# Performance work log

Hardware: AMD Instinct MI355X
Metric: run time of the kernel (lower is better)

Reference implementation:

```python
import jax, jax.numpy as jnp
import numpy as np
from jax import lax

B, D, H, W = 4, 32, 256, 256
ALPHA = 4.0     # init arg alpha
KFRAMES = 4.0   # self.K = alpha
EPS_BN = 1e-5

def FT2d(a):
    return jnp.fft.fft2(a, axes=(-2, -1))

def iFT2d(a):
    return jnp.fft.ifft2(a, axes=(-2, -1))

def forward_proj(field, otf):
    # field [B,D,H,W] real, otf [B,D,H,W] complex -> min-max scaled |holo| [B,1,H,W]
    Fholo = jnp.sum(FT2d(field.astype(jnp.complex64)) * otf, axis=1, keepdims=True)
    holo = jnp.abs(iFT2d(Fholo))
    mn = holo.min(axis=(-2, -1), keepdims=True)
    mx = holo.max(axis=(-2, -1), keepdims=True)
    return (holo - mn) / (mx - mn)

def back_proj(holo, otf):
    # holo [B,1,H,W] real -> real field [B,D,H,W]; broadcasting over depth == tile+FFT
    Fh = FT2d(holo.astype(jnp.complex64))
    return jnp.real(iFT2d(Fh * jnp.conj(otf)))

def cbl(xin, w, g, b, act):
    y = lax.conv_general_dilated(xin, w, (1, 1), 'SAME',
                                 dimension_numbers=('NCHW', 'OIHW', 'NCHW'))
    m = y.mean(axis=(0, 2, 3), keepdims=True)
    v = y.var(axis=(0, 2, 3), keepdims=True)  # biased var, torch BN training-mode
    y = (y - m) * lax.rsqrt(v + EPS_BN) * g[None, :, None, None] + b[None, :, None, None]
    return jax.nn.leaky_relu(y, 0.01) if act else y

def resblock(xin, wa, ga, ba, wb, gb, bb):
    h = cbl(cbl(xin, wa, ga, ba, True), wb, gb, bb, False)
    return jax.nn.leaky_relu(xin + h, 0.01)

def plholonet_forward(phi, z, u1, u2, otf, K1f, rho1, rho2, soft_thr, p):
    # ---- X update: FFT-domain proximal solve ----
    x1 = phi - u1
    x2 = z - u2
    n = rho1 * back_proj(x1, otf) + rho2 * x2
    d = (rho2 + jnp.abs(otf) ** 2 * rho1).astype(jnp.complex64)
    x = jnp.real(iFT2d(FT2d(n.astype(jnp.complex64)) / d))
    # ---- Phi update: vectorized 30-step masked bisection ----
    phi_tilde = forward_proj(x, otf) + u1
    K0 = 1.0 - K1f
    c = ALPHA / KFRAMES
    def func(y):
        return c * (K0 - K1f / (jnp.exp(c * y) - 1.0)) + rho1 * (y - phi_tilde)
    ind0_init = K1f == 0
    phimin = jnp.full_like(phi_tilde, 1e-5)
    phimax = jnp.full_like(phi_tilde, 100.0)
    phiave = 0.5 * (phimin + phimax)
    def step(carry, _):
        pmin, pmax, pave, ind0 = carry
        ind1 = jnp.logical_not(ind0)
        t = func(pave)
        pmin = jnp.where((t > 0) & ind1, pave, pmin)
        pmax = jnp.where((t < 0) & ind1, pave, pmax)
        ind0 = ind0 | ((t == 0) & ind1)
        pave = jnp.where(jnp.logical_not(ind0), 0.5 * (pmin + pmax), pave)
        return (pmin, pmax, pave, ind0), None
    (_, _, phiave, _), _ = lax.scan(step, (phimin, phimax, phiave, ind0_init), None, length=30)
    phi_next = jnp.where(ind0_init, phi_tilde - K0 / rho1, phiave)
    # ---- Z update: denoiser with symmetry loss ----
    z_tilde = x + u2
    h1 = resblock(z_tilde, p['w1a'], p['g1a'], p['b1a'], p['w1b'], p['g1b'], p['b1b'])
    h1_thr = jnp.sign(h1) * jax.nn.relu(jnp.abs(h1) - soft_thr)
    z_next = resblock(h1_thr, p['w2a'], p['g2a'], p['b2a'], p['w2b'], p['g2b'], p['b2b'])
    x_fb = resblock(h1, p['w2a'], p['g2a'], p['b2a'], p['w2b'], p['g2b'], p['b2b'])
    stage_symloss = x_fb - z_tilde
    # ---- dual updates ----
    u1_next = u1 + phi_next - forward_proj(x, otf)
    u2_next = u2 + z_next - x
    return (x, phi_next, z_next, u1_next, u2_next, stage_symloss)

def setup_inputs() -> dict:
    key = jax.random.key(0)
    ks = jax.random.split(key, 16)
    f = jnp.float32
    inp = dict(
        x=jax.random.normal(ks[0], (B, D, H, W), f),
        phi=jax.random.uniform(ks[1], (B, 1, H, W), dtype=f),
        z=jax.random.normal(ks[2], (B, D, H, W), f) * 0.1,
        u1=jax.random.uniform(ks[3], (B, 1, H, W), dtype=f) * 0.1,
        u2=jax.random.uniform(ks[4], (B, D, H, W), dtype=f) * 0.1,
        otf_real=jax.random.normal(ks[5], (B, D, H, W), f) * 0.5,
        otf_imag=jax.random.normal(ks[6], (B, D, H, W), f) * 0.5,
        K1=jax.random.randint(ks[7], (B, 1, H, W), 0, 5, jnp.int32),
        rho1=jnp.array([0.7], f),
        rho2=jnp.array([0.5], f),
        soft_thr=jnp.array([0.01], f),
    )
    for i, sfx in enumerate(['1a', '1b', '2a', '2b']):
        inp['w' + sfx] = jax.random.normal(ks[8 + i], (D, D, 3, 3), f) * 0.05
        inp['g' + sfx] = jnp.ones((D,), f)
        inp['b' + sfx] = jnp.zeros((D,), f)
    return inp

def reference(x, phi, z, u1, u2, otf_real, otf_imag, K1, rho1, rho2, soft_thr,
              w1a, g1a, b1a, w1b, g1b, b1b, w2a, g2a, b2a, w2b, g2b, b2b):
    # note: the torch forward immediately overwrites its `x` argument via X_update,
    # so the input x is unused (kept in the signature for interface faithfulness).
    otf = (otf_real + 1j * otf_imag).astype(jnp.complex64)
    K1f = K1.astype(jnp.float32)
    p = dict(w1a=w1a, g1a=g1a, b1a=b1a, w1b=w1b, g1b=g1b, b1b=b1b,
             w2a=w2a, g2a=g2a, b2a=b2a, w2b=w2b, g2b=g2b, b2b=b2b)
    return plholonet_forward(phi, z, u1, u2, otf, K1f, rho1, rho2, soft_thr, p)
```

## Files before the change

### kernel.cpp

```cpp
#include <hip/hip_runtime.h>
#include <math.h>

#define WDIM 256
#define HW   65536

struct cplx { float x, y; };
__device__ __forceinline__ cplx cmul(cplx a, cplx b){ return {a.x*b.x - a.y*b.y, a.x*b.y + a.y*b.x}; }
__device__ __forceinline__ cplx cadd(cplx a, cplx b){ return {a.x+b.x, a.y+b.y}; }
__device__ __forceinline__ cplx csub(cplx a, cplx b){ return {a.x-b.x, a.y-b.y}; }
__device__ __forceinline__ void swapc(cplx& a, cplx& b){ cplx t=a; a=b; b=t; }

typedef __attribute__((ext_vector_type(8))) short short8;
typedef __attribute__((ext_vector_type(4))) float float4v;

__device__ __forceinline__ unsigned short f2bf(float f){
  unsigned int u = __float_as_uint(f);
  unsigned int r = (u + 0x7FFFu + ((u >> 16) & 1u)) >> 16;
  return (unsigned short)r;
}
__device__ __forceinline__ float bf2f(unsigned short h){
  return __uint_as_float(((unsigned int)h) << 16);
}

template<bool INV>
__device__ __forceinline__ void fft16(cplx v[16]) {
  const float C16[8] = {1.f, 0.9238795325112867f, 0.7071067811865476f, 0.3826834323650898f,
                        0.f, -0.3826834323650898f, -0.7071067811865476f, -0.9238795325112867f};
  const float S16[8] = {0.f, 0.3826834323650898f, 0.7071067811865476f, 0.9238795325112867f,
                        1.f, 0.9238795325112867f, 0.7071067811865476f, 0.3826834323650898f};
  swapc(v[1], v[8]); swapc(v[2], v[4]); swapc(v[3], v[12]);
  swapc(v[5], v[10]); swapc(v[7], v[14]); swapc(v[11], v[13]);
  #pragma unroll
  for (int s = 1; s <= 4; ++s) {
    const int m = 1 << s, half = m >> 1, step = 16 >> s;
    #pragma unroll
    for (int k = 0; k < 16; k += m) {
      #pragma unroll
      for (int j = 0; j < half; ++j) {
        cplx w = {C16[j*step], INV ? S16[j*step] : -S16[j*step]};
        cplx t = cmul(w, v[k+j+half]);
        v[k+j+half] = csub(v[k+j], t);
        v[k+j]      = cadd(v[k+j], t);
      }
    }
  }
}

template<bool INV>
__device__ void fft256_16(cplx v[16], int t, cplx* Yu) {
  fft16<INV>(v);
  float ang = (INV ? 6.283185307179586f : -6.283185307179586f) * (float)t * (1.0f/256.0f);
  float sn, cs; sincosf(ang, &sn, &cs);
  cplx wstep = {cs, sn}, w = {1.f, 0.f};
  #pragma unroll
  for (int c = 0; c < 16; ++c) { v[c] = cmul(v[c], w); w = cmul(w, wstep); }
  __syncthreads();
  #pragma unroll
  for (int c = 0; c < 16; ++c) Yu[t*17 + c] = v[c];
  __syncthreads();
  cplx z[16];
  #pragma unroll
  for (int b = 0; b < 16; ++b) z[b] = Yu[b*17 + t];
  fft16<INV>(z);
  #pragma unroll
  for (int d = 0; d < 16; ++d) v[d] = z[d];
  __syncthreads();
}

__global__ __launch_bounds__(256) void k_row_fwd_sub(const float* __restrict__ a,
                                                     const float* __restrict__ b,
                                                     cplx* __restrict__ out) {
  __shared__ cplx Y[16*280];
  int unit = threadIdx.x >> 4, t = threadIdx.x & 15;
  size_t base = (size_t)blockIdx.y*HW + (size_t)(blockIdx.x*16 + unit)*WDIM;
  cplx v[16];
  #pragma unroll
  for (int i = 0; i < 16; ++i) { size_t idx = base + i*16 + t; v[i] = {a[idx] - b[idx], 0.f}; }
  fft256_16<false>(v, t, Y + unit*280);
  #pragma unroll
  for (int d = 0; d < 16; ++d) out[base + t + 16*d] = v[d];
}

__global__ __launch_bounds__(256) void k_row_fwd_sub_p(const float* __restrict__ a,
                                                       const float* __restrict__ b,
                                                       cplx* __restrict__ out) {
  __shared__ cplx Y[16*280];
  int unit = threadIdx.x >> 4, t = threadIdx.x & 15;
  int bp = blockIdx.y; int bb = bp >> 4, p = bp & 15;
  size_t rowoff = (size_t)(blockIdx.x*16 + unit)*WDIM;
  size_t base0 = ((size_t)(bb*32 + 2*p))*HW + rowoff;
  size_t base1 = base0 + HW;
  size_t baseo = (size_t)bp*HW + rowoff;
  cplx v[16];
  #pragma unroll
  for (int i = 0; i < 16; ++i) {
    size_t o = i*16 + t;
    v[i] = {a[base0+o] - b[base0+o], a[base1+o] - b[base1+o]};
  }
  fft256_16<false>(v, t, Y + unit*280);
  #pragma unroll
  for (int d = 0; d < 16; ++d) out[baseo + t + 16*d] = v[d];
}

__global__ __launch_bounds__(256) void k_row_inv(const cplx* __restrict__ in,
                                                 cplx* __restrict__ out) {
  __shared__ cplx Y[16*280];
  int unit = threadIdx.x >> 4, t = threadIdx.x & 15;
  size_t base = (size_t)blockIdx.y*HW + (size_t)(blockIdx.x*16 + unit)*WDIM;
  cplx v[16];
  #pragma unroll
  for (int i = 0; i < 16; ++i) v[i] = in[base + i*16 + t];
  fft256_16<true>(v, t, Y + unit*280);
  #pragma unroll
  for (int d = 0; d < 16; ++d) out[base + t + 16*d] = {v[d].x*(1.f/256.f), v[d].y*(1.f/256.f)};
}

template<bool INV>
__device__ void col_core(const cplx* __restrict__ in, cplx* lds, cplx v[16], size_t planeBase) {
  int tid = threadIdx.x;
  #pragma unroll
  for (int i = 0; i < 16; ++i) {
    int idx = tid + 256*i; int h = idx >> 4, w = idx & 15;
    lds[h*17 + w] = in[planeBase + (size_t)h*WDIM + w];
  }
  __syncthreads();
  int u = tid >> 4, t = tid & 15;
  cplx vv[16];
  #pragma unroll
  for (int a = 0; a < 16; ++a) vv[a] = lds[(16*a + t)*17 + u];
  fft256_16<INV>(vv, t, lds + u*280);
  #pragma unroll
  for (int d = 0; d < 16; ++d) v[d] = vv[d];
}

__global__ __launch_bounds__(256) void k_col_fwd(cplx* __restrict__ buf) {
  __shared__ cplx lds[4480];
  size_t planeBase = (size_t)blockIdx.y*HW + blockIdx.x*16;
  cplx v[16];
  col_core<false>(buf, lds, v, planeBase);
  int u = threadIdx.x >> 4, t = threadIdx.x & 15;
  #pragma unroll
  for (int d = 0; d < 16; ++d) lds[(t + 16*d)*17 + u] = v[d];
  __syncthreads();
  int tid = threadIdx.x;
  #pragma unroll
  for (int i = 0; i < 16; ++i) {
    int idx = tid + 256*i; int h = idx >> 4, w = idx & 15;
    buf[planeBase + (size_t)h*WDIM + w] = lds[h*17 + w];
  }
}

__global__ __launch_bounds__(256) void k_col_inv_xzt_p(const cplx* __restrict__ in,
                                                       const float* __restrict__ u2,
                                                       float* __restrict__ xout,
                                                       unsigned short* __restrict__ ztcl) {
  __shared__ cplx lds[4480];
  int bp = blockIdx.y; int bb = bp >> 4, p = bp & 15;
  size_t planeBase = (size_t)bp*HW + blockIdx.x*16;
  cplx v[16];
  col_core<true>(in, lds, v, planeBase);
  int u = threadIdx.x >> 4, t = threadIdx.x & 15;
  #pragma unroll
  for (int d = 0; d < 16; ++d) lds[(t + 16*d)*17 + u] = {v[d].x*(1.f/256.f), v[d].y*(1.f/256.f)};
  __syncthreads();
  int tid = threadIdx.x;
  size_t out0 = ((size_t)(bb*32 + 2*p))*HW + blockIdx.x*16;
  size_t out1 = out0 + HW;
  #pragma unroll
  for (int i = 0; i < 16; ++i) {
    int idx = tid + 256*i; int h = idx >> 4, w = idx & 15;
    cplx val = lds[h*17 + w];
    size_t g0 = out0 + (size_t)h*WDIM + w;
    size_t g1 = out1 + (size_t)h*WDIM + w;
    float zt0 = val.x + u2[g0];
    float zt1 = val.y + u2[g1];
    xout[g0] = val.x;
    xout[g1] = val.y;
    int pix = (h << 8) + (blockIdx.x << 4) + w;
    unsigned int pk = ((unsigned int)f2bf(zt1) << 16) | (unsigned int)f2bf(zt0);
    *(unsigned int*)(ztcl + ((((size_t)(bb << 16)) + pix) << 5) + 2*p) = pk;
  }
}

__global__ __launch_bounds__(256) void k_col_inv_abs(const cplx* __restrict__ in,
                                                     float* __restrict__ holo,
                                                     float* __restrict__ partials) {
  __shared__ cplx lds[4480];
  float* ldsf = (float*)lds;
  size_t planeBase = (size_t)blockIdx.y*HW + blockIdx.x*16;
  cplx v[16];
  col_core<true>(in, lds, v, planeBase);
  int u = threadIdx.x >> 4, t = threadIdx.x & 15;
  #pragma unroll
  for (int d = 0; d < 16; ++d) {
    float re = v[d].x*(1.f/256.f), im = v[d].y*(1.f/256.f);
    ldsf[(t + 16*d)*17 + u] = sqrtf(re*re + im*im);
  }
  __syncthreads();
  int tid = threadIdx.x;
  float mn = 1e30f, mx = -1e30f;
  #pragma unroll
  for (int i = 0; i < 16; ++i) {
    int idx = tid + 256*i; int h = idx >> 4, w = idx & 15;
    float val = ldsf[h*17 + w];
    holo[planeBase + (size_t)h*WDIM + w] = val;
    mn = fminf(mn, val); mx = fmaxf(mx, val);
  }
  __syncthreads();
  #pragma unroll
  for (int s = 1; s < 64; s <<= 1) { mn = fminf(mn, __shfl_xor(mn, s)); mx = fmaxf(mx, __shfl_xor(mx, s)); }
  if ((tid & 63) == 0) { ldsf[(tid>>6)*2] = mn; ldsf[(tid>>6)*2 + 1] = mx; }
  __syncthreads();
  if (tid == 0) {
    float a = fminf(fminf(ldsf[0], ldsf[2]), fminf(ldsf[4], ldsf[6]));
    float b = fmaxf(fmaxf(ldsf[1], ldsf[3]), fmaxf(ldsf[5], ldsf[7]));
    partials[(blockIdx.y*16 + blockIdx.x)*2]     = a;
    partials[(blockIdx.y*16 + blockIdx.x)*2 + 1] = b;
  }
}

__global__ __launch_bounds__(64) void k_mm_reduce(const float* __restrict__ partials,
                                                  float* __restrict__ minmax) {
  int t = threadIdx.x; int b = t >> 4, i = t & 15;
  float mn = partials[(b*16 + i)*2], mx = partials[(b*16 + i)*2 + 1];
  #pragma unroll
  for (int s = 1; s < 16; s <<= 1) { mn = fminf(mn, __shfl_xor(mn, s)); mx = fmaxf(mx, __shfl_xor(mx, s)); }
  if (i == 0) { minmax[b*2] = mn; minmax[b*2 + 1] = mx; }
}

__global__ __launch_bounds__(256) void k_combine_hf(const cplx* __restrict__ P,
                                                    cplx* __restrict__ Q,
                                                    const cplx* __restrict__ X1F,
                                                    const float* __restrict__ otr,
                                                    const float* __restrict__ oti,
                                                    const float* __restrict__ r1p,
                                                    const float* __restrict__ r2p,
                                                    cplx* __restrict__ HF) {
  int j = blockIdx.x*256 + threadIdx.x;
  int b = j / 33024;
  int r = j - b*33024;
  int kh = r >> 8, kw = r & 255;
  if ((kh == 0 || kh == 128) && kw > 128) return;
  int k  = (kh << 8) | kw;
  int k2 = ((((256 - kh) & 255)) << 8) | ((256 - kw) & 255);
  float rho1 = r1p[0], rho2 = r2p[0];
  cplx A  = X1F[(b << 16) | k];
  cplx Am = X1F[(b << 16) | k2];
  float hfr = 0.f, hfi = 0.f, hfr2 = 0.f, hfi2 = 0.f;
  #pragma unroll 1
  for (int p = 0; p < 16; ++p) {
    int pb = (b*16 + p) << 16;
    cplx Pk = P[pb | k], Pm = P[pb | k2];
    float Zr[2], Zi[2];
    Zr[0] = 0.5f*(Pk.x + Pm.x); Zi[0] = 0.5f*(Pk.y - Pm.y);
    Zr[1] = 0.5f*(Pk.y + Pm.y); Zi[1] = 0.5f*(Pm.x - Pk.x);
    float Xr[2], Xi[2];
    #pragma unroll
    for (int dd = 0; dd < 2; ++dd) {
      int db = (b*32 + 2*p + dd) << 16;
      float or1 = otr[db | k],  oi1 = oti[db | k];
      float or2 = otr[db | k2], oi2 = oti[db | k2];
      float Gr = 0.5f*(A.x*or1 + A.y*oi1 + Am.x*or2 + Am.y*oi2);
      float Gi = 0.5f*(A.y*or1 - A.x*oi1 + Am.x*oi2 - Am.y*or2);
      float di = 0.5f*(1.f/(rho2 + rho1*(or1*or1 + oi1*oi1))
                     + 1.f/(rho2 + rho1*(or2*or2 + oi2*oi2)));
      float xr = (rho1*Gr + rho2*Zr[dd])*di;
      float xi = (rho1*Gi + rho2*Zi[dd])*di;
      Xr[dd] = xr; Xi[dd] = xi;
      hfr  += xr*or1 - xi*oi1;
      hfi  += xr*oi1 + xi*or1;
      hfr2 += xr*or2 + xi*oi2;
      hfi2 += xr*oi2 - xi*or2;
    }
    Q[pb | k]  = {Xr[0] - Xi[1], Xi[0] + Xr[1]};
    Q[pb | k2] = {Xr[0] + Xi[1], Xr[1] - Xi[0]};
  }
  HF[(b << 16) | k]  = {hfr,  hfi};
  HF[(b << 16) | k2] = {hfr2, hfi2};
}

__global__ __launch_bounds__(256) void k_bisect(const float* __restrict__ holo,
                                                const float* __restrict__ minmax,
                                                const float* __restrict__ u1,
                                                const int* __restrict__ K1,
                                                const float* __restrict__ r1p,
                                                float* __restrict__ phi_out,
                                                float* __restrict__ u1_out) {
  int i = blockIdx.x*256 + threadIdx.x;
  int b = i >> 16;
  float mn = minmax[2*b], mx = minmax[2*b + 1];
  float fp = (holo[i] - mn) / (mx - mn);
  float pt = fp + u1[i];
  float K1f = (float)K1[i];
  float K0 = 1.f - K1f;
  float rho1 = r1p[0];
  bool ind0i = (K1f == 0.f);
  bool ind0 = ind0i;
  float pmin = 1e-5f, pmax = 100.f, pave = 0.5f*(pmin + pmax);
  #pragma unroll 1
  for (int it = 0; it < 30; ++it) {
    float e = expf(pave);
    float t = (K0 - K1f/(e - 1.f)) + rho1*(pave - pt);
    bool ind1 = !ind0;
    if (t > 0.f && ind1) pmin = pave;
    if (t < 0.f && ind1) pmax = pave;
    ind0 = ind0 || (t == 0.f && ind1);
    if (!ind0) pave = 0.5f*(pmin + pmax);
  }
  float pn = ind0i ? (pt - K0/rho1) : pave;
  phi_out[i] = pn;
  u1_out[i]  = u1[i] + pn - fp;
}

__global__ __launch_bounds__(256) void k_wprep(const float* __restrict__ w1a,
                                               const float* __restrict__ w1b,
                                               const float* __restrict__ w2a,
                                               const float* __restrict__ w2b,
                                               unsigned short* __restrict__ Ap) {
  int idx = blockIdx.x*256 + threadIdx.x;
  if (idx >= 4*9216) return;
  int wsel = idx / 9216, r = idx - wsel*9216;
  const float* w = wsel==0 ? w1a : wsel==1 ? w1b : wsel==2 ? w2a : w2b;
  int tap = r / 1024, r2 = r - tap*1024, oc = r2 >> 5, ic = r2 & 31;
  Ap[idx] = f2bf(w[(oc*32 + ic)*9 + tap]);
}

#define CONV_R 4
__global__ __launch_bounds__(256, 4) void k_conv(const unsigned short* __restrict__ inCL,
                                                 const unsigned short* __restrict__ Aprep,
                                                 unsigned short* __restrict__ outCL,
                                                 float* __restrict__ part,
                                                 int mode,
                                                 const float* __restrict__ scsh,
                                                 const float* __restrict__ thrp) {
  __shared__ unsigned short tile[6*66*32];
  __shared__ float sred[4][16][2];
  int tid = threadIdx.x;
  int bx = blockIdx.x, by = blockIdx.y, bz = blockIdx.z;
  int w0 = bx*64, h0 = by*CONV_R;
  float thr = (mode == 2) ? thrp[0] : 0.f;

  for (int idx = tid; idx < 6*264; idx += 256) {
    int lrow = idx/264, rem = idx - lrow*264;
    int lcol = rem >> 2, m = rem & 3;
    int grow = h0 - 1 + lrow, gcol = w0 - 1 + lcol;
    uint4 val = {0,0,0,0};
    if (grow >= 0 && grow < 256 && gcol >= 0 && gcol < 256) {
      uint4 raw = *(const uint4*)(inCL + (((size_t)(bz<<16) + (grow<<8) + gcol)<<5) + m*8);
      if (mode == 0) val = raw;
      else {
        unsigned short h8[8]; *(uint4*)h8 = raw;
        #pragma unroll
        for (int j = 0; j < 8; ++j) {
          float v = bf2f(h8[j]);
          if (mode == 1) { int ic = m*8+j; v = v*scsh[ic] + scsh[32+ic]; v = v > 0.f ? v : 0.01f*v; }
          else { float s = fabsf(v) - thr; s = s > 0.f ? s : 0.f; v = copysignf(s, v); }
          h8[j] = f2bf(v);
        }
        val = *(uint4*)h8;
      }
    }
    *(uint4*)&tile[(size_t)idx*8] = val;
  }

  int lane = tid & 63, w = tid >> 6;
  int q = lane >> 4, ln = lane & 15;
  int ocH = w & 1, s0 = w >> 1;
  short8 afrag[9];
  #pragma unroll
  for (int t = 0; t < 9; ++t)
    afrag[t] = *(const short8*)(Aprep + ((t*32 + ocH*16 + ln)*32 + q*8));
  __syncthreads();

  float sacc[4] = {0,0,0,0}, s2acc[4] = {0,0,0,0};
  #pragma unroll
  for (int r = 0; r < CONV_R; ++r) {
    #pragma unroll
    for (int si = 0; si < 2; ++si) {
      int s = s0 + si*2;
      float4v acc = {0.f, 0.f, 0.f, 0.f};
      #pragma unroll
      for (int t = 0; t < 9; ++t) {
        int dy = t/3, dx = t - dy*3;
        int lrow = r + dy, lcol = s*16 + ln + dx;
        const short8 bfrag = *(const short8*)&tile[(lrow*66 + lcol)*32 + q*8];
        acc = __builtin_amdgcn_mfma_f32_16x16x32_bf16(afrag[t], bfrag, acc, 0, 0, 0);
      }
      int px = w0 + s*16 + ln, row = h0 + r;
      size_t obase = ((((size_t)(bz<<16) + (row<<8) + px))<<5) + ocH*16 + q*4;
      unsigned short o4[4];
      #pragma unroll
      for (int u = 0; u < 4; ++u) { o4[u] = f2bf(acc[u]); sacc[u] += acc[u]; s2acc[u] += acc[u]*acc[u]; }
      *(uint2*)(outCL + obase) = *(uint2*)o4;
    }
  }

  #pragma unroll
  for (int u = 0; u < 4; ++u) {
    float a = sacc[u], b2 = s2acc[u];
    #pragma unroll
    for (int mq = 1; mq < 16; mq <<= 1) { a += __shfl_xor(a, mq); b2 += __shfl_xor(b2, mq); }
    if (ln == 0) { sred[w][q*4+u][0] = a; sred[w][q*4+u][1] = b2; }
  }
  __syncthreads();
  if (tid < 64) {
    int ocH2 = tid >> 5, i16 = (tid >> 1) & 15, st = tid & 1;
    float tot = sred[ocH2][i16][st] + sred[ocH2+2][i16][st];
    int oc = ocH2*16 + i16;
    int blk = ((bz<<6) + by)*4 + bx;
    part[(oc*2+st)*1024 + blk] = tot;
  }
}

__global__ __launch_bounds__(256) void k_finstats2(const float* __restrict__ part,
                                                   const float* __restrict__ g,
                                                   const float* __restrict__ beta,
                                                   float* __restrict__ SS) {
  __shared__ float red[8];
  int oc = blockIdx.x, t = threadIdx.x;
  const float* ps = part + oc*2048;
  float s  = ps[t] + ps[t+256] + ps[t+512] + ps[t+768];
  float s2 = ps[1024+t] + ps[1280+t] + ps[1536+t] + ps[1792+t];
  #pragma unroll
  for (int m = 1; m < 64; m <<= 1) { s += __shfl_xor(s, m); s2 += __shfl_xor(s2, m); }
  if ((t & 63) == 0) { red[(t>>6)*2] = s; red[(t>>6)*2+1] = s2; }
  __syncthreads();
  if (t == 0) {
    float S  = red[0] + red[2] + red[4] + red[6];
    float S2 = red[1] + red[3] + red[5] + red[7];
    const float N = 262144.f;
    float mean = S / N;
    float var  = S2 / N - mean*mean;
    float sc = g[oc] * rsqrtf(var + 1e-5f);
    SS[oc] = sc; SS[32+oc] = beta[oc] - mean*sc;
  }
}

__global__ __launch_bounds__(256) void k_h1cl(const unsigned short* __restrict__ zt,
                                              const unsigned short* __restrict__ c2,
                                              const float* __restrict__ SS,
                                              unsigned short* __restrict__ h1) {
  int idx = blockIdx.x*256 + threadIdx.x;
  int cg = idx & 3;
  uint4 za = *(const uint4*)(zt + (size_t)idx*8);
  uint4 ca = *(const uint4*)(c2 + (size_t)idx*8);
  unsigned short zs[8], cs[8], os[8];
  *(uint4*)zs = za; *(uint4*)cs = ca;
  #pragma unroll
  for (int j = 0; j < 8; ++j) {
    int c = cg*8 + j;
    float v = bf2f(zs[j]) + bf2f(cs[j])*SS[c] + SS[32+c];
    v = v > 0.f ? v : 0.01f*v;
    os[j] = f2bf(v);
  }
  *(uint4*)(h1 + (size_t)idx*8) = *(uint4*)os;
}

__global__ __launch_bounds__(256) void k_finalAB(const unsigned short* __restrict__ h1,
                                                 const unsigned short* __restrict__ c4,
                                                 const unsigned short* __restrict__ c6,
                                                 const unsigned short* __restrict__ ztcl,
                                                 const float* __restrict__ SS4,
                                                 const float* __restrict__ SS6,
                                                 const float* __restrict__ thrp,
                                                 const float* __restrict__ u2,
                                                 const float* __restrict__ x,
                                                 float* __restrict__ zout,
                                                 float* __restrict__ u2out,
                                                 float* __restrict__ symout) {
  __shared__ float zT[32*66];
  __shared__ float sT[32*66];
  int tid = threadIdx.x;
  size_t b = blockIdx.y;
  int px0 = blockIdx.x*64;
  float thr = thrp[0];
  int px = tid >> 2, cg = tid & 3;
  size_t cbase = ((((b<<16) + px0 + px))<<5) + cg*8;
  uint4 ha = *(const uint4*)(h1 + cbase);
  uint4 c4a = *(const uint4*)(c4 + cbase);
  uint4 c6a = *(const uint4*)(c6 + cbase);
  uint4 za = *(const uint4*)(ztcl + cbase);
  unsigned short hs[8], c4s[8], c6s[8], zs[8];
  *(uint4*)hs = ha; *(uint4*)c4s = c4a; *(uint4*)c6s = c6a; *(uint4*)zs = za;
  #pragma unroll
  for (int j = 0; j < 8; ++j) {
    int c = cg*8+j;
    float hv = bf2f(hs[j]);
    float s = fabsf(hv) - thr; s = s > 0.f ? s : 0.f;
    float th = copysignf(s, hv);
    float zv = th + bf2f(c4s[j])*SS4[c] + SS4[32+c];
    zT[c*66 + px] = zv > 0.f ? zv : 0.01f*zv;
    float xv = hv + bf2f(c6s[j])*SS6[c] + SS6[32+c];
    xv = xv > 0.f ? xv : 0.01f*xv;
    sT[c*66 + px] = xv - bf2f(zs[j]);
  }
  __syncthreads();
  #pragma unroll
  for (int i = 0; i < 2; ++i) {
    int ch = tid + i*256; int c = ch >> 4, p4 = (ch & 15)*4;
    size_t g = ((b*32 + c)<<16) + px0 + p4;
    float4 uv = *(const float4*)(u2 + g);
    float4 xv = *(const float4*)(x + g);
    float4 zv = { zT[c*66+p4], zT[c*66+p4+1], zT[c*66+p4+2], zT[c*66+p4+3] };
    float4 un = { uv.x+zv.x-xv.x, uv.y+zv.y-xv.y, uv.z+zv.z-xv.z, uv.w+zv.w-xv.w };
    float4 sv = { sT[c*66+p4], sT[c*66+p4+1], sT[c*66+p4+2], sT[c*66+p4+3] };
    *(float4*)(zout + g) = zv;
    *(float4*)(u2out + g) = un;
    *(float4*)(symout + g) = sv;
  }
}

extern "C" void kernel_launch(void* const* d_in, const int* in_sizes, int n_in,
                              void* d_out, int out_size, void* d_ws, size_t ws_size,
                              hipStream_t stream) {
  const float* phi  = (const float*)d_in[1];
  const float* z    = (const float*)d_in[2];
  const float* u1   = (const float*)d_in[3];
  const float* u2   = (const float*)d_in[4];
  const float* otr  = (const float*)d_in[5];
  const float* oti  = (const float*)d_in[6];
  const int*   K1   = (const int*)d_in[7];
  const float* rho1 = (const float*)d_in[8];
  const float* rho2 = (const float*)d_in[9];
  const float* sthr = (const float*)d_in[10];
  const float* w1a = (const float*)d_in[11];
  const float* g1a = (const float*)d_in[12];
  const float* b1a = (const float*)d_in[13];
  const float* w1b = (const float*)d_in[14];
  const float* g1b = (const float*)d_in[15];
  const float* b1b = (const float*)d_in[16];
  const float* w2a = (const float*)d_in[17];
  const float* g2a = (const float*)d_in[18];
  const float* b2a = (const float*)d_in[19];
  const float* w2b = (const float*)d_in[20];
  const float* g2b = (const float*)d_in[21];
  const float* b2b = (const float*)d_in[22];

  float* out = (float*)d_out;
  float* x_out   = out;
  float* phi_out = out + 8388608;
  float* z_out   = out + 8650752;
  float* u1_out  = out + 17039360;
  float* u2_out  = out + 17301504;
  float* sym_out = out + 25690112;

  char* ws = (char*)d_ws;
  cplx*  P     = (cplx*)ws;
  cplx*  Q     = (cplx*)(ws + 33554432);
  cplx*  X1R   = (cplx*)(ws + 67108864);
  cplx*  HFT   = (cplx*)(ws + 69206016);
  float* holo  = (float*)(ws + 71303168);
  float* partmm= (float*)(ws + 72351744);
  float* mm    = (float*)(ws + 72355840);

  unsigned short* Ap    = (unsigned short*)(ws + 71303168);
  float*          part  = (float*)(ws + 71434240);
  float*          SSb   = (float*)(ws + 71696384);
  unsigned short* ZTcl  = (unsigned short*)(ws + 33554432);
  unsigned short* H1cl  = (unsigned short*)(ws + 50331648);
  unsigned short* C4cl  = (unsigned short*)(ws + 0);
  unsigned short* C2cl  = (unsigned short*)(ws + 16777216);
  unsigned short* C6cl  = (unsigned short*)(ws + 16777216);
  unsigned short* C135  = (unsigned short*)z_out;
  cplx* W2 = (cplx*)z_out;

  k_row_fwd_sub  <<<dim3(16, 4),  256, 0, stream>>>(phi, u1, X1R);
  k_col_fwd      <<<dim3(16, 4),  256, 0, stream>>>(X1R);
  k_row_fwd_sub_p<<<dim3(16, 64), 256, 0, stream>>>(z, u2, P);
  k_col_fwd      <<<dim3(16, 64), 256, 0, stream>>>(P);
  k_combine_hf   <<<516, 256, 0, stream>>>(P, Q, X1R, otr, oti, rho1, rho2, HFT);
  k_row_inv      <<<dim3(16, 4),  256, 0, stream>>>(HFT, X1R);
  k_col_inv_abs  <<<dim3(16, 4),  256, 0, stream>>>(X1R, holo, partmm);
  k_mm_reduce    <<<1, 64, 0, stream>>>(partmm, mm);
  k_row_inv      <<<dim3(16, 64), 256, 0, stream>>>(Q, W2);
  k_col_inv_xzt_p<<<dim3(16, 64), 256, 0, stream>>>(W2, u2, x_out, ZTcl);
  k_bisect<<<1024, 256, 0, stream>>>(holo, mm, u1, K1, rho1, phi_out, u1_out);

  k_wprep<<<144, 256, 0, stream>>>(w1a, w1b, w2a, w2b, Ap);

  dim3 cg(4, 64, 4);
  k_conv<<<cg, 256, 0, stream>>>(ZTcl, Ap + 0,      C135, part, 0, SSb,       sthr);
  k_finstats2<<<32, 256, 0, stream>>>(part, g1a, b1a, SSb + 0);
  k_conv<<<cg, 256, 0, stream>>>(C135, Ap + 9216,   C2cl, part, 1, SSb + 0,   sthr);
  k_finstats2<<<32, 256, 0, stream>>>(part, g1b, b1b, SSb + 64);
  k_h1cl<<<4096, 256, 0, stream>>>(ZTcl, C2cl, SSb + 64, H1cl);

  k_conv<<<cg, 256, 0, stream>>>(H1cl, Ap + 18432,  C135, part, 2, SSb,       sthr);
  k_finstats2<<<32, 256, 0, stream>>>(part, g2a, b2a, SSb + 128);
  k_conv<<<cg, 256, 0, stream>>>(C135, Ap + 27648,  C4cl, part, 1, SSb + 128, sthr);
  k_finstats2<<<32, 256, 0, stream>>>(part, g2b, b2b, SSb + 192);

  k_conv<<<cg, 256, 0, stream>>>(H1cl, Ap + 18432,  C135, part, 0, SSb,       sthr);
  k_finstats2<<<32, 256, 0, stream>>>(part, g2a, b2a, SSb + 256);
  k_conv<<<cg, 256, 0, stream>>>(C135, Ap + 27648,  C6cl, part, 1, SSb + 256, sthr);
  k_finstats2<<<32, 256, 0, stream>>>(part, g2b, b2b, SSb + 320);

  k_finalAB<<<dim3(1024, 4), 256, 0, stream>>>(H1cl, C4cl, C6cl, ZTcl,
                                               SSb + 192, SSb + 320, sthr, u2, x_out,
                                               z_out, u2_out, sym_out);
}
```

Measured before the change: 556.2 us.

## Batch FFT launches, pack real FFTs in pairs, fuse the twin resblock convolutions

Merges the small phi-u1 FFT path into the batched z-u2 FFT kernels through extra grid rows, so each FFT stage is one launch. The two real planes are packed into one complex FFT and separated afterwards with conjugate symmetry in the combine kernel. The two resblock-2 branches (thresholded and raw input) share one tile load and compute in k_conv35, and their second convolutions and BN stats run in paired kernels. This cuts launch count and lets several small grids fill the GPU together. It uses more LDS and registers per block and needs extra workspace buffers.

New measurement: 501.1 us. -9.9%, faster.

```diff
diff --git a/kernel.cpp b/kernel.cpp
--- a/kernel.cpp
+++ b/kernel.cpp
@@ -67,52 +67,40 @@
   __syncthreads();
 }
 
-__global__ __launch_bounds__(256) void k_row_fwd_sub(const float* __restrict__ a,
+__global__ __launch_bounds__(256) void k_row_fwd_all(const float* __restrict__ a,
                                                      const float* __restrict__ b,
-                                                     cplx* __restrict__ out) {
+                                                     const float* __restrict__ sa,
+                                                     const float* __restrict__ sb,
+                                                     cplx* __restrict__ P,
+                                                     cplx* __restrict__ XS) {
   __shared__ cplx Y[16*280];
   int unit = threadIdx.x >> 4, t = threadIdx.x & 15;
-  size_t base = (size_t)blockIdx.y*HW + (size_t)(blockIdx.x*16 + unit)*WDIM;
-  cplx v[16];
-  #pragma unroll
-  for (int i = 0; i < 16; ++i) { size_t idx = base + i*16 + t; v[i] = {a[idx] - b[idx], 0.f}; }
-  fft256_16<false>(v, t, Y + unit*280);
-  #pragma unroll
-  for (int d = 0; d < 16; ++d) out[base + t + 16*d] = v[d];
-}
-
-__global__ __launch_bounds__(256) void k_row_fwd_sub_p(const float* __restrict__ a,
-                                                       const float* __restrict__ b,
-                                                       cplx* __restrict__ out) {
-  __shared__ cplx Y[16*280];
-  int unit = threadIdx.x >> 4, t = threadIdx.x & 15;
-  int bp = blockIdx.y; int bb = bp >> 4, p = bp & 15;
+  int bp = blockIdx.y;
   size_t rowoff = (size_t)(blockIdx.x*16 + unit)*WDIM;
-  size_t base0 = ((size_t)(bb*32 + 2*p))*HW + rowoff;
+  const float *pa, *pb;
+  size_t base0, baseo_rel;
+  cplx* outb;
+  if (bp < 64) {
+    int bb = bp >> 4, p = bp & 15;
+    pa = a; pb = b;
+    base0 = ((size_t)(bb*32 + 2*p))*HW + rowoff;
+    outb = P; baseo_rel = (size_t)bp*HW + rowoff;
+  } else {
+    int pp = bp - 64;
+    pa = sa; pb = sb;
+    base0 = ((size_t)(2*pp))*HW + rowoff;
+    outb = XS; baseo_rel = (size_t)pp*HW + rowoff;
+  }
   size_t base1 = base0 + HW;
-  size_t baseo = (size_t)bp*HW + rowoff;
   cplx v[16];
   #pragma unroll
   for (int i = 0; i < 16; ++i) {
     size_t o = i*16 + t;
-    v[i] = {a[base0+o] - b[base0+o], a[base1+o] - b[base1+o]};
+    v[i] = {pa[base0+o] - pb[base0+o], pa[base1+o] - pb[base1+o]};
   }
   fft256_16<false>(v, t, Y + unit*280);
   #pragma unroll
-  for (int d = 0; d < 16; ++d) out[baseo + t + 16*d] = v[d];
-}
-
-__global__ __launch_bounds__(256) void k_row_inv(const cplx* __restrict__ in,
-                                                 cplx* __restrict__ out) {
-  __shared__ cplx Y[16*280];
-  int unit = threadIdx.x >> 4, t = threadIdx.x & 15;
-  size_t base = (size_t)blockIdx.y*HW + (size_t)(blockIdx.x*16 + unit)*WDIM;
-  cplx v[16];
-  #pragma unroll
-  for (int i = 0; i < 16; ++i) v[i] = in[base + i*16 + t];
-  fft256_16<true>(v, t, Y + unit*280);
-  #pragma unroll
-  for (int d = 0; d < 16; ++d) out[base + t + 16*d] = {v[d].x*(1.f/256.f), v[d].y*(1.f/256.f)};
+  for (int d = 0; d < 16; ++d) outb[baseo_rel + t + 16*d] = v[d];
 }
 
 template<bool INV>
@@ -133,9 +121,12 @@
   for (int d = 0; d < 16; ++d) v[d] = vv[d];
 }
 
-__global__ __launch_bounds__(256) void k_col_fwd(cplx* __restrict__ buf) {
+__global__ __launch_bounds__(256) void k_col_fwd_all(cplx* __restrict__ P,
+                                                     cplx* __restrict__ XS) {
   __shared__ cplx lds[4480];
-  size_t planeBase = (size_t)blockIdx.y*HW + blockIdx.x*16;
+  int y = blockIdx.y;
+  cplx* buf = (y < 64) ? (P + (size_t)y*HW) : (XS + (size_t)(y-64)*HW);
+  size_t planeBase = blockIdx.x*16;
   cplx v[16];
   col_core<false>(buf, lds, v, planeBase);
   int u = threadIdx.x >> 4, t = threadIdx.x & 15;
@@ -150,72 +141,91 @@
   }
 }
 
-__global__ __launch_bounds__(256) void k_col_inv_xzt_p(const cplx* __restrict__ in,
-                                                       const float* __restrict__ u2,
-                                                       float* __restrict__ xout,
-                                                       unsigned short* __restrict__ ztcl) {
-  __shared__ cplx lds[4480];
-  int bp = blockIdx.y; int bb = bp >> 4, p = bp & 15;
-  size_t planeBase = (size_t)bp*HW + blockIdx.x*16;
+__global__ __launch_bounds__(256) void k_row_inv_all(const cplx* __restrict__ Q,
+                                                     const cplx* __restrict__ HFT,
+                                                     cplx* __restrict__ W2,
+                                                     cplx* __restrict__ XS) {
+  __shared__ cplx Y[16*280];
+  int unit = threadIdx.x >> 4, t = threadIdx.x & 15;
+  int y = blockIdx.y;
+  const cplx* inb;  cplx* outb;
+  if (y < 64) { inb = Q + (size_t)y*HW; outb = W2 + (size_t)y*HW; }
+  else        { inb = HFT + (size_t)(y-64)*HW; outb = XS + (size_t)(y-64)*HW; }
+  size_t base = (size_t)(blockIdx.x*16 + unit)*WDIM;
   cplx v[16];
-  col_core<true>(in, lds, v, planeBase);
-  int u = threadIdx.x >> 4, t = threadIdx.x & 15;
-  #pragma unroll
-  for (int d = 0; d < 16; ++d) lds[(t + 16*d)*17 + u] = {v[d].x*(1.f/256.f), v[d].y*(1.f/256.f)};
-  __syncthreads();
-  int tid = threadIdx.x;
-  size_t out0 = ((size_t)(bb*32 + 2*p))*HW + blockIdx.x*16;
-  size_t out1 = out0 + HW;
-  #pragma unroll
-  for (int i = 0; i < 16; ++i) {
-    int idx = tid + 256*i; int h = idx >> 4, w = idx & 15;
-    cplx val = lds[h*17 + w];
-    size_t g0 = out0 + (size_t)h*WDIM + w;
-    size_t g1 = out1 + (size_t)h*WDIM + w;
-    float zt0 = val.x + u2[g0];
-    float zt1 = val.y + u2[g1];
-    xout[g0] = val.x;
-    xout[g1] = val.y;
-    int pix = (h << 8) + (blockIdx.x << 4) + w;
-    unsigned int pk = ((unsigned int)f2bf(zt1) << 16) | (unsigned int)f2bf(zt0);
-    *(unsigned int*)(ztcl + ((((size_t)(bb << 16)) + pix) << 5) + 2*p) = pk;
-  }
-}
-
-__global__ __launch_bounds__(256) void k_col_inv_abs(const cplx* __restrict__ in,
+  #pragma unroll
+  for (int i = 0; i < 16; ++i) v[i] = inb[base + i*16 + t];
+  fft256_16<true>(v, t, Y + unit*280);
+  #pragma unroll
+  for (int d = 0; d < 16; ++d) outb[base + t + 16*d] = {v[d].x*(1.f/256.f), v[d].y*(1.f/256.f)};
+}
+
+__global__ __launch_bounds__(256) void k_col_inv_all(const cplx* __restrict__ W2,
+                                                     const cplx* __restrict__ XS,
+                                                     const float* __restrict__ u2,
+                                                     float* __restrict__ xout,
+                                                     unsigned short* __restrict__ ztcl,
                                                      float* __restrict__ holo,
                                                      float* __restrict__ partials) {
   __shared__ cplx lds[4480];
-  float* ldsf = (float*)lds;
-  size_t planeBase = (size_t)blockIdx.y*HW + blockIdx.x*16;
-  cplx v[16];
-  col_core<true>(in, lds, v, planeBase);
-  int u = threadIdx.x >> 4, t = threadIdx.x & 15;
-  #pragma unroll
-  for (int d = 0; d < 16; ++d) {
-    float re = v[d].x*(1.f/256.f), im = v[d].y*(1.f/256.f);
-    ldsf[(t + 16*d)*17 + u] = sqrtf(re*re + im*im);
-  }
-  __syncthreads();
+  int y = blockIdx.y;
   int tid = threadIdx.x;
-  float mn = 1e30f, mx = -1e30f;
-  #pragma unroll
-  for (int i = 0; i < 16; ++i) {
-    int idx = tid + 256*i; int h = idx >> 4, w = idx & 15;
-    float val = ldsf[h*17 + w];
-    holo[planeBase + (size_t)h*WDIM + w] = val;
-    mn = fminf(mn, val); mx = fmaxf(mx, val);
-  }
-  __syncthreads();
-  #pragma unroll
-  for (int s = 1; s < 64; s <<= 1) { mn = fminf(mn, __shfl_xor(mn, s)); mx = fmaxf(mx, __shfl_xor(mx, s)); }
-  if ((tid & 63) == 0) { ldsf[(tid>>6)*2] = mn; ldsf[(tid>>6)*2 + 1] = mx; }
-  __syncthreads();
-  if (tid == 0) {
-    float a = fminf(fminf(ldsf[0], ldsf[2]), fminf(ldsf[4], ldsf[6]));
-    float b = fmaxf(fmaxf(ldsf[1], ldsf[3]), fmaxf(ldsf[5], ldsf[7]));
-    partials[(blockIdx.y*16 + blockIdx.x)*2]     = a;
-    partials[(blockIdx.y*16 + blockIdx.x)*2 + 1] = b;
+  if (y < 64) {
+    int bb = y >> 4, p = y & 15;
+    cplx v[16];
+    col_core<true>(W2 + (size_t)y*HW, lds, v, blockIdx.x*16);
+    int u = tid >> 4, t = tid & 15;
+    #pragma unroll
+    for (int d = 0; d < 16; ++d) lds[(t + 16*d)*17 + u] = {v[d].x*(1.f/256.f), v[d].y*(1.f/256.f)};
+    __syncthreads();
+    size_t out0 = ((size_t)(bb*32 + 2*p))*HW + blockIdx.x*16;
+    size_t out1 = out0 + HW;
+    #pragma unroll
+    for (int i = 0; i < 16; ++i) {
+      int idx = tid + 256*i; int h = idx >> 4, w = idx & 15;
+      cplx val = lds[h*17 + w];
+      size_t g0 = out0 + (size_t)h*WDIM + w;
+      size_t g1 = out1 + (size_t)h*WDIM + w;
+      float zt0 = val.x + u2[g0];
+      float zt1 = val.y + u2[g1];
+      xout[g0] = val.x;
+      xout[g1] = val.y;
+      int pix = (h << 8) + (blockIdx.x << 4) + w;
+      unsigned int pk = ((unsigned int)f2bf(zt1) << 16) | (unsigned int)f2bf(zt0);
+      *(unsigned int*)(ztcl + ((((size_t)(bb << 16)) + pix) << 5) + 2*p) = pk;
+    }
+  } else {
+    int py = y - 64;
+    float* ldsf = (float*)lds;
+    cplx v[16];
+    col_core<true>(XS + (size_t)py*HW, lds, v, blockIdx.x*16);
+    int u = tid >> 4, t = tid & 15;
+    #pragma unroll
+    for (int d = 0; d < 16; ++d) {
+      float re = v[d].x*(1.f/256.f), im = v[d].y*(1.f/256.f);
+      ldsf[(t + 16*d)*17 + u] = sqrtf(re*re + im*im);
+    }
+    __syncthreads();
+    float mn = 1e30f, mx = -1e30f;
+    size_t planeBase = (size_t)py*HW + blockIdx.x*16;
+    #pragma unroll
+    for (int i = 0; i < 16; ++i) {
+      int idx = tid + 256*i; int h = idx >> 4, w = idx & 15;
+      float val = ldsf[h*17 + w];
+      holo[planeBase + (size_t)h*WDIM + w] = val;
+      mn = fminf(mn, val); mx = fmaxf(mx, val);
+    }
+    __syncthreads();
+    #pragma unroll
+    for (int s = 1; s < 64; s <<= 1) { mn = fminf(mn, __shfl_xor(mn, s)); mx = fmaxf(mx, __shfl_xor(mx, s)); }
+    if ((tid & 63) == 0) { ldsf[(tid>>6)*2] = mn; ldsf[(tid>>6)*2 + 1] = mx; }
+    __syncthreads();
+    if (tid == 0) {
+      float a = fminf(fminf(ldsf[0], ldsf[2]), fminf(ldsf[4], ldsf[6]));
+      float b = fmaxf(fmaxf(ldsf[1], ldsf[3]), fmaxf(ldsf[5], ldsf[7]));
+      partials[(py*16 + blockIdx.x)*2]     = a;
+      partials[(py*16 + blockIdx.x)*2 + 1] = b;
+    }
   }
 }
 
@@ -230,7 +240,7 @@
 
 __global__ __launch_bounds__(256) void k_combine_hf(const cplx* __restrict__ P,
                                                     cplx* __restrict__ Q,
-                                                    const cplx* __restrict__ X1F,
+                                                    const cplx* __restrict__ XS,
                                                     const float* __restrict__ otr,
                                                     const float* __restrict__ oti,
                                                     const float* __restrict__ r1p,
@@ -244,8 +254,12 @@
   int k  = (kh << 8) | kw;
   int k2 = ((((256 - kh) & 255)) << 8) | ((256 - kw) & 255);
   float rho1 = r1p[0], rho2 = r2p[0];
-  cplx A  = X1F[(b << 16) | k];
-  cplx Am = X1F[(b << 16) | k2];
+  int c = b >> 1, par = b & 1;
+  cplx Sk = XS[(c << 16) | k], Sm = XS[(c << 16) | k2];
+  cplx A;
+  if (par == 0) A = {0.5f*(Sk.x + Sm.x), 0.5f*(Sk.y - Sm.y)};
+  else          A = {0.5f*(Sk.y + Sm.y), 0.5f*(Sm.x - Sk.x)};
+  cplx Am = {A.x, -A.y};
   float hfr = 0.f, hfi = 0.f, hfr2 = 0.f, hfi2 = 0.f;
   #pragma unroll 1
   for (int p = 0; p < 16; ++p) {
@@ -338,7 +352,6 @@
   int tid = threadIdx.x;
   int bx = blockIdx.x, by = blockIdx.y, bz = blockIdx.z;
   int w0 = bx*64, h0 = by*CONV_R;
-  float thr = (mode == 2) ? thrp[0] : 0.f;
 
   for (int idx = tid; idx < 6*264; idx += 256) {
     int lrow = idx/264, rem = idx - lrow*264;
@@ -353,8 +366,7 @@
         #pragma unroll
         for (int j = 0; j < 8; ++j) {
           float v = bf2f(h8[j]);
-          if (mode == 1) { int ic = m*8+j; v = v*scsh[ic] + scsh[32+ic]; v = v > 0.f ? v : 0.01f*v; }
-          else { float s = fabsf(v) - thr; s = s > 0.f ? s : 0.f; v = copysignf(s, v); }
+          int ic = m*8+j; v = v*scsh[ic] + scsh[32+ic]; v = v > 0.f ? v : 0.01f*v;
           h8[j] = f2bf(v);
         }
         val = *(uint4*)h8;
@@ -412,12 +424,228 @@
   }
 }
 
+__global__ __launch_bounds__(256, 3) void k_conv35(const unsigned short* __restrict__ inCL,
+                                                   const unsigned short* __restrict__ Aprep,
+                                                   unsigned short* __restrict__ outT,
+                                                   unsigned short* __restrict__ outR,
+                                                   float* __restrict__ partT,
+                                                   float* __restrict__ partR,
+                                                   const float* __restrict__ thrp) {
+  __shared__ unsigned short tileR[6*66*32];
+  __shared__ unsigned short tileT[6*66*32];
+  __shared__ float sredT[4][16][2];
+  __shared__ float sredR[4][16][2];
+  int tid = threadIdx.x;
+  int bx = blockIdx.x, by = blockIdx.y, bz = blockIdx.z;
+  int w0 = bx*64, h0 = by*CONV_R;
+  float thr = thrp[0];
+
+  for (int idx = tid; idx < 6*264; idx += 256) {
+    int lrow = idx/264, rem = idx - lrow*264;
+    int lcol = rem >> 2, m = rem & 3;
+    int grow = h0 - 1 + lrow, gcol = w0 - 1 + lcol;
+    uint4 raw = {0,0,0,0}, thrv = {0,0,0,0};
+    if (grow >= 0 && grow < 256 && gcol >= 0 && gcol < 256) {
+      raw = *(const uint4*)(inCL + (((size_t)(bz<<16) + (grow<<8) + gcol)<<5) + m*8);
+      unsigned short h8[8], t8[8]; *(uint4*)h8 = raw;
+      #pragma unroll
+      for (int j = 0; j < 8; ++j) {
+        float v = bf2f(h8[j]);
+        float s = fabsf(v) - thr; s = s > 0.f ? s : 0.f;
+        t8[j] = f2bf(copysignf(s, v));
+      }
+      thrv = *(uint4*)t8;
+    }
+    *(uint4*)&tileR[(size_t)idx*8] = raw;
+    *(uint4*)&tileT[(size_t)idx*8] = thrv;
+  }
+
+  int lane = tid & 63, w = tid >> 6;
+  int q = lane >> 4, ln = lane & 15;
+  int ocH = w & 1, s0 = w >> 1;
+  short8 afrag[9];
+  #pragma unroll
+  for (int t = 0; t < 9; ++t)
+    afrag[t] = *(const short8*)(Aprep + ((t*32 + ocH*16 + ln)*32 + q*8));
+  __syncthreads();
+
+  float saT[4] = {0,0,0,0}, s2T[4] = {0,0,0,0};
+  float saR[4] = {0,0,0,0}, s2R[4] = {0,0,0,0};
+  #pragma unroll
+  for (int r = 0; r < CONV_R; ++r) {
+    #pragma unroll
+    for (int si = 0; si < 2; ++si) {
+      int s = s0 + si*2;
+      float4v accT = {0.f,0.f,0.f,0.f}, accR = {0.f,0.f,0.f,0.f};
+      #pragma unroll
+      for (int t = 0; t < 9; ++t) {
+        int dy = t/3, dx = t - dy*3;
+        int lrow = r + dy, lcol = s*16 + ln + dx;
+        size_t off = ((size_t)(lrow*66 + lcol))*32 + q*8;
+        const short8 bT = *(const short8*)&tileT[off];
+        accT = __builtin_amdgcn_mfma_f32_16x16x32_bf16(afrag[t], bT, accT, 0, 0, 0);
+        const short8 bR = *(const short8*)&tileR[off];
+        accR = __builtin_amdgcn_mfma_f32_16x16x32_bf16(afrag[t], bR, accR, 0, 0, 0);
+      }
+      int px = w0 + s*16 + ln, row = h0 + r;
+      size_t obase = ((((size_t)(bz<<16) + (row<<8) + px))<<5) + ocH*16 + q*4;
+      unsigned short oT[4], oR[4];
+      #pragma unroll
+      for (int u = 0; u < 4; ++u) {
+        oT[u] = f2bf(accT[u]); saT[u] += accT[u]; s2T[u] += accT[u]*accT[u];
+        oR[u] = f2bf(accR[u]); saR[u] += accR[u]; s2R[u] += accR[u]*accR[u];
+      }
+      *(uint2*)(outT + obase) = *(uint2*)oT;
+      *(uint2*)(outR + obase) = *(uint2*)oR;
+    }
+  }
+
+  #pragma unroll
+  for (int u = 0; u < 4; ++u) {
+    float aT = saT[u], bT2 = s2T[u], aR = saR[u], bR2 = s2R[u];
+    #pragma unroll
+    for (int mq = 1; mq < 16; mq <<= 1) {
+      aT += __shfl_xor(aT, mq); bT2 += __shfl_xor(bT2, mq);
+      aR += __shfl_xor(aR, mq); bR2 += __shfl_xor(bR2, mq);
+    }
+    if (ln == 0) {
+      sredT[w][q*4+u][0] = aT; sredT[w][q*4+u][1] = bT2;
+      sredR[w][q*4+u][0] = aR; sredR[w][q*4+u][1] = bR2;
+    }
+  }
+  __syncthreads();
+  if (tid < 64) {
+    int ocH2 = tid >> 5, i16 = (tid >> 1) & 15, st = tid & 1;
+    int oc = ocH2*16 + i16;
+    int blk = ((bz<<6) + by)*4 + bx;
+    partT[(oc*2+st)*1024 + blk] = sredT[ocH2][i16][st] + sredT[ocH2+2][i16][st];
+    partR[(oc*2+st)*1024 + blk] = sredR[ocH2][i16][st] + sredR[ocH2+2][i16][st];
+  }
+}
+
+__global__ __launch_bounds__(256, 4) void k_conv_pair(const unsigned short* __restrict__ inA,
+                                                      const unsigned short* __restrict__ inB,
+                                                      unsigned short* __restrict__ outA,
+                                                      unsigned short* __restrict__ outB,
+                                                      float* __restrict__ partA,
+                                                      float* __restrict__ partB,
+                                                      const float* __restrict__ ssA,
+                                                      const float* __restrict__ ssB,
+                                                      const unsigned short* __restrict__ Aprep) {
+  __shared__ unsigned short tile[6*66*32];
+  __shared__ float sred[4][16][2];
+  int tid = threadIdx.x;
+  int bx = blockIdx.x, by = blockIdx.y;
+  int half = blockIdx.z >> 2, bz = blockIdx.z & 3;
+  const unsigned short* inCL = half ? inB : inA;
+  unsigned short* outCL = half ? outB : outA;
+  const float* scsh = half ? ssB : ssA;
+  float* part = half ? partB : partA;
+  int w0 = bx*64, h0 = by*CONV_R;
+
+  for (int idx = tid; idx < 6*264; idx += 256) {
+    int lrow = idx/264, rem = idx - lrow*264;
+    int lcol = rem >> 2, m = rem & 3;
+    int grow = h0 - 1 + lrow, gcol = w0 - 1 + lcol;
+    uint4 val = {0,0,0,0};
+    if (grow >= 0 && grow < 256 && gcol >= 0 && gcol < 256) {
+      uint4 raw = *(const uint4*)(inCL + (((size_t)(bz<<16) + (grow<<8) + gcol)<<5) + m*8);
+      unsigned short h8[8]; *(uint4*)h8 = raw;
+      #pragma unroll
+      for (int j = 0; j < 8; ++j) {
+        float v = bf2f(h8[j]);
+        int ic = m*8+j; v = v*scsh[ic] + scsh[32+ic]; v = v > 0.f ? v : 0.01f*v;
+        h8[j] = f2bf(v);
+      }
+      val = *(uint4*)h8;
+    }
+    *(uint4*)&tile[(size_t)idx*8] = val;
+  }
+
+  int lane = tid & 63, w = tid >> 6;
+  int q = lane >> 4, ln = lane & 15;
+  int ocH = w & 1, s0 = w >> 1;
+  short8 afrag[9];
+  #pragma unroll
+  for (int t = 0; t < 9; ++t)
+    afrag[t] = *(const short8*)(Aprep + ((t*32 + ocH*16 + ln)*32 + q*8));
+  __syncthreads();
+
+  float sacc[4] = {0,0,0,0}, s2acc[4] = {0,0,0,0};
+  #pragma unroll
+  for (int r = 0; r < CONV_R; ++r) {
+    #pragma unroll
+    for (int si = 0; si < 2; ++si) {
+      int s = s0 + si*2;
+      float4v acc = {0.f, 0.f, 0.f, 0.f};
+      #pragma unroll
+      for (int t = 0; t < 9; ++t) {
+        int dy = t/3, dx = t - dy*3;
+        int lrow = r + dy, lcol = s*16 + ln + dx;
+        const short8 bfrag = *(const short8*)&tile[(lrow*66 + lcol)*32 + q*8];
+        acc = __builtin_amdgcn_mfma_f32_16x16x32_bf16(afrag[t], bfrag, acc, 0, 0, 0);
+      }
+      int px = w0 + s*16 + ln, row = h0 + r;
+      size_t obase = ((((size_t)(bz<<16) + (row<<8) + px))<<5) + ocH*16 + q*4;
+      unsigned short o4[4];
+      #pragma unroll
+      for (int u = 0; u < 4; ++u) { o4[u] = f2bf(acc[u]); sacc[u] += acc[u]; s2acc[u] += acc[u]*acc[u]; }
+      *(uint2*)(outCL + obase) = *(uint2*)o4;
+    }
+  }
+
+  #pragma unroll
+  for (int u = 0; u < 4; ++u) {
+    float a = sacc[u], b2 = s2acc[u];
+    #pragma unroll
+    for (int mq = 1; mq < 16; mq <<= 1) { a += __shfl_xor(a, mq); b2 += __shfl_xor(b2, mq); }
+    if (ln == 0) { sred[w][q*4+u][0] = a; sred[w][q*4+u][1] = b2; }
+  }
+  __syncthreads();
+  if (tid < 64) {
+    int ocH2 = tid >> 5, i16 = (tid >> 1) & 15, st = tid & 1;
+    float tot = sred[ocH2][i16][st] + sred[ocH2+2][i16][st];
+    int oc = ocH2*16 + i16;
+    int blk = ((bz<<6) + by)*4 + bx;
+    part[(oc*2+st)*1024 + blk] = tot;
+  }
+}
+
 __global__ __launch_bounds__(256) void k_finstats2(const float* __restrict__ part,
                                                    const float* __restrict__ g,
                                                    const float* __restrict__ beta,
                                                    float* __restrict__ SS) {
   __shared__ float red[8];
   int oc = blockIdx.x, t = threadIdx.x;
+  const float* ps = part + oc*2048;
+  float s  = ps[t] + ps[t+256] + ps[t+512] + ps[t+768];
+  float s2 = ps[1024+t] + ps[1280+t] + ps[1536+t] + ps[1792+t];
+  #pragma unroll
+  for (int m = 1; m < 64; m <<= 1) { s += __shfl_xor(s, m); s2 += __shfl_xor(s2, m); }
+  if ((t & 63) == 0) { red[(t>>6)*2] = s; red[(t>>6)*2+1] = s2; }
+  __syncthreads();
+  if (t == 0) {
+    float S  = red[0] + red[2] + red[4] + red[6];
+    float S2 = red[1] + red[3] + red[5] + red[7];
+    const float N = 262144.f;
+    float mean = S / N;
+    float var  = S2 / N - mean*mean;
+    float sc = g[oc] * rsqrtf(var + 1e-5f);
+    SS[oc] = sc; SS[32+oc] = beta[oc] - mean*sc;
+  }
+}
+
+__global__ __launch_bounds__(256) void k_finstats_dual(const float* __restrict__ pA,
+                                                       const float* __restrict__ pB,
+                                                       const float* __restrict__ g,
+                                                       const float* __restrict__ beta,
+                                                       float* __restrict__ SSa,
+                                                       float* __restrict__ SSc) {
+  __shared__ float red[8];
+  int bxi = blockIdx.x;
+  const float* part = bxi < 32 ? pA : pB;
+  float* SS = bxi < 32 ? SSa : SSc;
+  int oc = bxi & 31, t = threadIdx.x;
   const float* ps = part + oc*2048;
   float s  = ps[t] + ps[t+256] + ps[t+512] + ps[t+768];
   float s2 = ps[1024+t] + ps[1280+t] + ps[1536+t] + ps[1792+t];
@@ -547,7 +775,7 @@
   char* ws = (char*)d_ws;
   cplx*  P     = (cplx*)ws;
   cplx*  Q     = (cplx*)(ws + 33554432);
-  cplx*  X1R   = (cplx*)(ws + 67108864);
+  cplx*  XS    = (cplx*)(ws + 67108864);
   cplx*  HFT   = (cplx*)(ws + 69206016);
   float* holo  = (float*)(ws + 71303168);
   float* partmm= (float*)(ws + 72351744);
@@ -555,45 +783,40 @@
 
   unsigned short* Ap    = (unsigned short*)(ws + 71303168);
   float*          part  = (float*)(ws + 71434240);
+  float*          partB = (float*)(ws + 69206016);
   float*          SSb   = (float*)(ws + 71696384);
   unsigned short* ZTcl  = (unsigned short*)(ws + 33554432);
   unsigned short* H1cl  = (unsigned short*)(ws + 50331648);
   unsigned short* C4cl  = (unsigned short*)(ws + 0);
   unsigned short* C2cl  = (unsigned short*)(ws + 16777216);
   unsigned short* C6cl  = (unsigned short*)(ws + 16777216);
-  unsigned short* C135  = (unsigned short*)z_out;
+  unsigned short* C135a = (unsigned short*)z_out;
+  unsigned short* C135b = (unsigned short*)((char*)z_out + 16777216);
   cplx* W2 = (cplx*)z_out;
 
-  k_row_fwd_sub  <<<dim3(16, 4),  256, 0, stream>>>(phi, u1, X1R);
-  k_col_fwd      <<<dim3(16, 4),  256, 0, stream>>>(X1R);
-  k_row_fwd_sub_p<<<dim3(16, 64), 256, 0, stream>>>(z, u2, P);
-  k_col_fwd      <<<dim3(16, 64), 256, 0, stream>>>(P);
-  k_combine_hf   <<<516, 256, 0, stream>>>(P, Q, X1R, otr, oti, rho1, rho2, HFT);
-  k_row_inv      <<<dim3(16, 4),  256, 0, stream>>>(HFT, X1R);
-  k_col_inv_abs  <<<dim3(16, 4),  256, 0, stream>>>(X1R, holo, partmm);
-  k_mm_reduce    <<<1, 64, 0, stream>>>(partmm, mm);
-  k_row_inv      <<<dim3(16, 64), 256, 0, stream>>>(Q, W2);
-  k_col_inv_xzt_p<<<dim3(16, 64), 256, 0, stream>>>(W2, u2, x_out, ZTcl);
+  k_row_fwd_all <<<dim3(16, 66), 256, 0, stream>>>(z, u2, phi, u1, P, XS);
+  k_col_fwd_all <<<dim3(16, 66), 256, 0, stream>>>(P, XS);
+  k_combine_hf  <<<516, 256, 0, stream>>>(P, Q, XS, otr, oti, rho1, rho2, HFT);
+  k_row_inv_all <<<dim3(16, 68), 256, 0, stream>>>(Q, HFT, W2, XS);
+  k_col_inv_all <<<dim3(16, 68), 256, 0, stream>>>(W2, XS, u2, x_out, ZTcl, holo, partmm);
+  k_mm_reduce   <<<1, 64, 0, stream>>>(partmm, mm);
   k_bisect<<<1024, 256, 0, stream>>>(holo, mm, u1, K1, rho1, phi_out, u1_out);
 
   k_wprep<<<144, 256, 0, stream>>>(w1a, w1b, w2a, w2b, Ap);
 
   dim3 cg(4, 64, 4);
-  k_conv<<<cg, 256, 0, stream>>>(ZTcl, Ap + 0,      C135, part, 0, SSb,       sthr);
+  k_conv<<<cg, 256, 0, stream>>>(ZTcl, Ap + 0,      C135a, part, 0, SSb,     sthr);
   k_finstats2<<<32, 256, 0, stream>>>(part, g1a, b1a, SSb + 0);
-  k_conv<<<cg, 256, 0, stream>>>(C135, Ap + 9216,   C2cl, part, 1, SSb + 0,   sthr);
+  k_conv<<<cg, 256, 0, stream>>>(C135a, Ap + 9216,  C2cl,  part, 1, SSb + 0, sthr);
   k_finstats2<<<32, 256, 0, stream>>>(part, g1b, b1b, SSb + 64);
   k_h1cl<<<4096, 256, 0, stream>>>(ZTcl, C2cl, SSb + 64, H1cl);
 
-  k_conv<<<cg, 256, 0, stream>>>(H1cl, Ap + 18432,  C135, part, 2, SSb,       sthr);
-  k_finstats2<<<32, 256, 0, stream>>>(part, g2a, b2a, SSb + 128);
-  k_conv<<<cg, 256, 0, stream>>>(C135, Ap + 27648,  C4cl, part, 1, SSb + 128, sthr);
-  k_finstats2<<<32, 256, 0, stream>>>(part, g2b, b2b, SSb + 192);
-
-  k_conv<<<cg, 256, 0, stream>>>(H1cl, Ap + 18432,  C135, part, 0, SSb,       sthr);
-  k_finstats2<<<32, 256, 0, stream>>>(part, g2a, b2a, SSb + 256);
-  k_conv<<<cg, 256, 0, stream>>>(C135, Ap + 27648,  C6cl, part, 1, SSb + 256, sthr);
-  k_finstats2<<<32, 256, 0, stream>>>(part, g2b, b2b, SSb + 320);
+  k_conv35<<<cg, 256, 0, stream>>>(H1cl, Ap + 18432, C135a, C135b, part, partB, sthr);
+  k_finstats_dual<<<64, 256, 0, stream>>>(part, partB, g2a, b2a, SSb + 128, SSb + 256);
+  k_conv_pair<<<dim3(4, 64, 8), 256, 0, stream>>>(C135a, C135b, C4cl, C6cl,
+                                                  part, partB, SSb + 128, SSb + 256,
+                                                  Ap + 27648);
+  k_finstats_dual<<<64, 256, 0, stream>>>(part, partB, g2b, b2b, SSb + 192, SSb + 320);
 
   k_finalAB<<<dim3(1024, 4), 256, 0, stream>>>(H1cl, C4cl, C6cl, ZTcl,
                                                SSb + 192, SSb + 320, sthr, u2, x_out,
```
